# Performance work log

Hardware: AMD Instinct MI355X
Metric: run time of the kernel (lower is better)

Reference implementation:

```python
import jax, jax.numpy as jnp
import numpy as np

# Hyperparameters (from init_kwargs)
D_MODEL = 1024
D_STATE = 64
HEADDIM = 64
MIMO_RANK = 2
CHUNK = 128
EXPAND = 2
D_INNER = EXPAND * D_MODEL            # 2048
NHEADS = D_INNER // HEADDIM           # 32
G = MIMO_RANK * D_STATE               # effective state channels per head = 128
D_CONV = 4
D_XBC = D_INNER + 2 * NHEADS * G      # conv channels
D_IN_PROJ = 2 * D_INNER + 2 * NHEADS * G + NHEADS  # [z, x, B, C, dt]


def rmsnorm(x, w, eps=1e-5):
    return x * w * jax.lax.rsqrt(jnp.mean(x * x, axis=-1, keepdims=True) + eps)


def setup_inputs() -> dict:
    key = jax.random.key(0)
    ks = jax.random.split(key, 8)
    B, L = 2, 2048
    x = jax.random.normal(ks[0], (B, L, D_MODEL), jnp.float32)
    norm_w = jnp.ones((D_MODEL,), jnp.float32)
    in_proj_w = jax.random.normal(ks[1], (D_IN_PROJ, D_MODEL), jnp.float32) * 0.02
    conv_w = jax.random.normal(ks[2], (D_XBC, D_CONV), jnp.float32) * 0.2
    conv_b = jnp.zeros((D_XBC,), jnp.float32)
    dt_bias = jax.random.uniform(ks[3], (NHEADS,), jnp.float32, minval=-4.0, maxval=-1.0)
    A_log = jnp.log(jax.random.uniform(ks[4], (NHEADS,), jnp.float32, minval=1.0, maxval=8.0))
    D_skip = jnp.ones((NHEADS,), jnp.float32)
    gnorm_w = jnp.ones((D_INNER,), jnp.float32)
    out_proj_w = jax.random.normal(ks[5], (D_MODEL, D_INNER), jnp.float32) * 0.02
    return dict(x=x, norm_w=norm_w, in_proj_w=in_proj_w, conv_w=conv_w, conv_b=conv_b,
                dt_bias=dt_bias, A_log=A_log, D_skip=D_skip, gnorm_w=gnorm_w,
                out_proj_w=out_proj_w)


def _mamba3(u, in_proj_w, conv_w, conv_b, dt_bias, A_log, D_skip, gnorm_w, out_proj_w):
    B, L, _ = u.shape
    H, P = NHEADS, HEADDIM
    nc = L // CHUNK

    zxbcdt = u @ in_proj_w.T                                   # (B,L,D_IN_PROJ)
    z, xbc, dt_raw = jnp.split(zxbcdt, [D_INNER, D_INNER + D_XBC], axis=-1)

    # causal depthwise conv (width D_CONV) + SiLU on [x, B, C]
    xp = jnp.pad(xbc, ((0, 0), (D_CONV - 1, 0), (0, 0)))
    conv = conv_b + sum(xp[:, k:k + L, :] * conv_w[:, k] for k in range(D_CONV))
    xbc = jax.nn.silu(conv)
    xh, Bm, Cm = jnp.split(xbc, [D_INNER, D_INNER + H * G], axis=-1)

    Xc = xh.reshape(B, nc, CHUNK, H, P)
    Bc = Bm.reshape(B, nc, CHUNK, H, G)
    Cc = Cm.reshape(B, nc, CHUNK, H, G)

    dt = jax.nn.softplus(dt_raw + dt_bias)                     # (B,L,H), positive
    A = -jnp.exp(A_log)                                        # (H,), negative
    dtc = dt.reshape(B, nc, CHUNK, H)
    a = dtc * A                                                # log decay, (B,nc,cs,H)
    cum = jnp.cumsum(a, axis=2)                                # inclusive cumsum within chunk

    # intra-chunk (quadratic, causal) part
    cumT = cum.transpose(0, 1, 3, 2)                           # (B,nc,H,cs)
    diff = cumT[..., :, None] - cumT[..., None, :]             # cum_l - cum_s
    mask = jnp.tril(jnp.ones((CHUNK, CHUNK), bool))
    decay = jnp.where(mask, jnp.exp(jnp.where(mask, diff, 0.0)), 0.0)
    dtT = dtc.transpose(0, 1, 3, 2)                            # (B,nc,H,cs)
    scores = jnp.einsum('bclhg,bcshg->bchls', Cc, Bc) * decay * dtT[:, :, :, None, :]
    Y_intra = jnp.einsum('bchls,bcshp->bclhp', scores, Xc)

    # inter-chunk state recurrence
    w = jnp.exp(cum[:, :, -1:, :] - cum) * dtc                 # (B,nc,cs,H)
    S = jnp.einsum('bcshg,bcshp->bchgp', Bc * w[..., None], Xc)  # chunk states
    dlast = jnp.exp(cum[:, :, -1, :])                          # (B,nc,H) total chunk decay

    def step(carry, inp):
        dl, s = inp
        return dl[:, :, None, None] * carry + s, carry

    init = jnp.zeros((B, H, G, P), u.dtype)
    _, Hprev = jax.lax.scan(step, init, (dlast.transpose(1, 0, 2), S.transpose(1, 0, 2, 3, 4)))
    Hprev = Hprev.transpose(1, 0, 2, 3, 4)                     # (B,nc,H,G,P) state before chunk
    Y_inter = jnp.einsum('bclhg,bchgp->bclhp', Cc * jnp.exp(cum)[..., None], Hprev)

    y = (Y_intra + Y_inter + D_skip[:, None] * Xc).reshape(B, L, D_INNER)
    y = rmsnorm(y * jax.nn.silu(z), gnorm_w)                   # gated RMSNorm
    return y @ out_proj_w.T


def reference(x, norm_w, in_proj_w, conv_w, conv_b, dt_bias, A_log, D_skip, gnorm_w, out_proj_w):
    # pre-norm residual wrapper
    return x + _mamba3(rmsnorm(x, norm_w), in_proj_w, conv_w, conv_b,
                       dt_bias, A_log, D_skip, gnorm_w, out_proj_w)
```

## Files before the change

### kernel.cpp

```cpp
#include <hip/hip_runtime.h>

typedef unsigned short u16;
typedef __attribute__((ext_vector_type(8))) short bf16x8;
typedef __attribute__((ext_vector_type(4))) float f32x4;

#define MFMA16(a,b,c) __builtin_amdgcn_mfma_f32_16x16x32_bf16(a,b,c,0,0,0)

#define DMODEL   1024
#define DINNER   2048
#define NHEADS   32
#define HEADDIM  64
#define GDIM     128
#define DXBC     10240
#define DPROJ    12320
#define CHUNK_L  128
#define NCHUNK   16
#define NROWS    4096

__device__ __forceinline__ float b2f(u16 u){ return __uint_as_float(((unsigned)u)<<16); }
__device__ __forceinline__ u16 f2b(float f){
  unsigned u = __float_as_uint(f);
  u += 0x7fffu + ((u>>16)&1u);
  return (u16)(u>>16);
}

__device__ __forceinline__ void gload_lds16(const void* g, void* l){
  __builtin_amdgcn_global_load_lds(
      (const __attribute__((address_space(1))) unsigned int*)g,
      (__attribute__((address_space(3))) unsigned int*)l, 16, 0, 0);
}

__global__ void k_f32_to_bf16_2(const float* __restrict__ s1, u16* __restrict__ d1, int n1,
                                const float* __restrict__ s2, u16* __restrict__ d2, int n2){
  int i = blockIdx.x*blockDim.x + threadIdx.x;
  int stride = gridDim.x*blockDim.x;
  int t1 = n1 >> 2, t2 = n2 >> 2;
  for (int j=i; j<t1+t2; j+=stride){
    const float4* sp; uint2* dp; int idx;
    if (j < t1){ sp = (const float4*)s1; dp = (uint2*)d1; idx = j; }
    else       { sp = (const float4*)s2; dp = (uint2*)d2; idx = j - t1; }
    float4 v = sp[idx];
    uint2 o;
    o.x = (unsigned)f2b(v.x) | ((unsigned)f2b(v.y)<<16);
    o.y = (unsigned)f2b(v.z) | ((unsigned)f2b(v.w)<<16);
    dp[idx] = o;
  }
}

__global__ __launch_bounds__(256) void k_rmsnorm_in(const float* __restrict__ x,
                                                    const float* __restrict__ w,
                                                    u16* __restrict__ u){
  int row = blockIdx.x, tid = threadIdx.x;
  float4 v = reinterpret_cast<const float4*>(x + (size_t)row*DMODEL)[tid];
  float ss = v.x*v.x + v.y*v.y + v.z*v.z + v.w*v.w;
  #pragma unroll
  for (int off=32; off>0; off>>=1) ss += __shfl_down(ss, off, 64);
  __shared__ float red[4];
  if ((tid&63)==0) red[tid>>6] = ss;
  __syncthreads();
  float tot = red[0]+red[1]+red[2]+red[3];
  float sc = rsqrtf(tot/(float)DMODEL + 1e-5f);
  float4 wv = reinterpret_cast<const float4*>(w)[tid];
  uint2 o;
  o.x = (unsigned)f2b(v.x*wv.x*sc) | ((unsigned)f2b(v.y*wv.y*sc)<<16);
  o.y = (unsigned)f2b(v.z*wv.z*sc) | ((unsigned)f2b(v.w*wv.w*sc)<<16);
  reinterpret_cast<uint2*>(u + (size_t)row*DMODEL)[tid] = o;
}

__global__ __launch_bounds__(512) void k_gemm1_8p(const u16* __restrict__ A,
                                                  const u16* __restrict__ W,
                                                  u16* __restrict__ zb,
                                                  u16* __restrict__ xbc){
  __shared__ __align__(16) u16 lds[65536];
  const int tid  = threadIdx.x;
  const int lane = tid & 63, w = tid >> 6;
  const int wr = w >> 2, wc = w & 3;
  int bid = blockIdx.x;
  int xcd = bid & 7, g = bid >> 3;
  int st  = xcd*6 + (g >> 4);
  int wi  = g & 15;
  int tm  = (st/12)*4 + (wi>>2);
  int tn  = (st%12)*4 + (wi&3);
  const int m0 = tm*256, n0 = tn*256;

  const int srow = w*8 + (lane>>3);
  const int scol = ((lane&7) ^ ((lane>>3)&7))*8;
  const u16* aS = A + (size_t)(m0 + srow)*DMODEL + scol;
  const u16* bS = W + (size_t)(n0 + srow)*DMODEL + scol;
  const int ldsw = w*512;

  const int rr = lane & 15, gq = lane >> 4;

  f32x4 acc[8][4];
  #pragma unroll
  for (int i=0;i<8;i++)
    #pragma unroll
    for (int j=0;j<4;j++) acc[i][j] = (f32x4){0,0,0,0};

  auto SU_A = [&](int kt, int j){
    gload_lds16(aS + (size_t)(j*64)*DMODEL + kt*64,
                lds + (kt&1)*32768 + j*4096 + ldsw);
  };
  auto SU_B = [&](int kt, int j){
    gload_lds16(bS + (size_t)(j*64)*DMODEL + kt*64,
                lds + (kt&1)*32768 + 16384 + j*4096 + ldsw);
  };

  SU_A(0,0); SU_A(0,2); SU_B(0,0); SU_B(0,2); SU_B(0,1); SU_B(0,3); SU_A(0,1); SU_A(0,3);
  asm volatile("s_waitcnt vmcnt(2)" ::: "memory");
  __builtin_amdgcn_s_barrier();
  __builtin_amdgcn_sched_barrier(0);

  for (int kt = 0; kt < 16; ++kt){
    const u16* bufA = lds + (kt&1)*32768;
    const u16* bufB = bufA + 16384;
    const bool stg = (kt < 15);
    bf16x8 af[4][2], bw0[2][2], bw1[2][2];

    auto RDA = [&](int ti, int ks)->bf16x8{
      int r = wr*128 + ti*16 + rr;
      int s = (ks*4 + gq) ^ (rr & 7);
      return *(const bf16x8*)&bufA[r*64 + s*8];
    };
    auto RDB = [&](int tj, int ks)->bf16x8{
      int r = wc*64 + tj*16 + rr;
      int s = (ks*4 + gq) ^ (rr & 7);
      return *(const bf16x8*)&bufB[r*64 + s*8];
    };

    #pragma unroll
    for (int ti=0;ti<4;ti++){ af[ti][0]=RDA(ti,0); af[ti][1]=RDA(ti,1); }
    #pragma unroll
    for (int tj=0;tj<2;tj++){ bw0[tj][0]=RDB(tj,0); bw0[tj][1]=RDB(tj,1); }
    if (stg){ SU_A(kt+1,0); SU_A(kt+1,2); }
    __builtin_amdgcn_s_barrier();
    asm volatile("s_waitcnt lgkmcnt(0)" ::: "memory");
    __builtin_amdgcn_sched_barrier(0);
    __builtin_amdgcn_s_setprio(1);
    #pragma unroll
    for (int ti=0;ti<4;ti++)
      #pragma unroll
      for (int tj=0;tj<2;tj++){
        acc[ti][tj] = MFMA16(af[ti][0], bw0[tj][0], acc[ti][tj]);
        acc[ti][tj] = MFMA16(af[ti][1], bw0[tj][1], acc[ti][tj]);
      }
    __builtin_amdgcn_s_setprio(0);
    __builtin_amdgcn_s_barrier();

    #pragma unroll
    for (int tj=0;tj<2;tj++){ bw1[tj][0]=RDB(tj+2,0); bw1[tj][1]=RDB(tj+2,1); }
    if (stg){ SU_B(kt+1,0); SU_B(kt+1,2); }
    __builtin_amdgcn_s_barrier();
    asm volatile("s_waitcnt lgkmcnt(0)" ::: "memory");
    __builtin_amdgcn_sched_barrier(0);
    __builtin_amdgcn_s_setprio(1);
    #pragma unroll
    for (int ti=0;ti<4;ti++)
      #pragma unroll
      for (int tj=0;tj<2;tj++){
        acc[ti][tj+2] = MFMA16(af[ti][0], bw1[tj][0], acc[ti][tj+2]);
        acc[ti][tj+2] = MFMA16(af[ti][1], bw1[tj][1], acc[ti][tj+2]);
      }
    __builtin_amdgcn_s_setprio(0);
    if (stg) asm volatile("s_waitcnt vmcnt(4)" ::: "memory");
    else     asm volatile("s_waitcnt vmcnt(0)" ::: "memory");
    __builtin_amdgcn_s_barrier();

    #pragma unroll
    for (int ti=0;ti<4;ti++){ af[ti][0]=RDA(ti+4,0); af[ti][1]=RDA(ti+4,1); }
    if (stg){ SU_B(kt+1,1); SU_B(kt+1,3); }
    __builtin_amdgcn_s_barrier();
    asm volatile("s_waitcnt lgkmcnt(0)" ::: "memory");
    __builtin_amdgcn_sched_barrier(0);
    __builtin_amdgcn_s_setprio(1);
    #pragma unroll
    for (int ti=0;ti<4;ti++)
      #pragma unroll
      for (int tj=0;tj<2;tj++){
        acc[4+ti][tj] = MFMA16(af[ti][0], bw0[tj][0], acc[4+ti][tj]);
        acc[4+ti][tj] = MFMA16(af[ti][1], bw0[tj][1], acc[4+ti][tj]);
      }
    __builtin_amdgcn_s_setprio(0);
    __builtin_amdgcn_s_barrier();

    if (stg){ SU_A(kt+1,1); SU_A(kt+1,3); }
    __builtin_amdgcn_s_barrier();
    __builtin_amdgcn_sched_barrier(0);
    __builtin_amdgcn_s_setprio(1);
    #pragma unroll
    for (int ti=0;ti<4;ti++)
      #pragma unroll
      for (int tj=0;tj<2;tj++){
        acc[4+ti][tj+2] = MFMA16(af[ti][0], bw1[tj][0], acc[4+ti][tj+2]);
        acc[4+ti][tj+2] = MFMA16(af[ti][1], bw1[tj][1], acc[4+ti][tj+2]);
      }
    __builtin_amdgcn_s_setprio(0);
    if (stg){
      asm volatile("s_waitcnt vmcnt(2)" ::: "memory");
      __builtin_amdgcn_s_barrier();
      __builtin_amdgcn_sched_barrier(0);
    }
  }

  const int row0 = m0 + wr*128 + (lane>>4)*4;
  const int colb = wc*64 + (lane&15);
  if (tn >= 8){
    const int cb = n0 - DINNER;
    #pragma unroll
    for (int ti=0;ti<8;ti++)
      #pragma unroll
      for (int tj=0;tj<4;tj++)
        #pragma unroll
        for (int q=0;q<4;q++)
          xbc[(size_t)(row0 + ti*16 + q)*DXBC + cb + colb + tj*16] = f2b(acc[ti][tj][q]);
  } else {
    #pragma unroll
    for (int ti=0;ti<8;ti++)
      #pragma unroll
      for (int tj=0;tj<4;tj++)
        #pragma unroll
        for (int q=0;q<4;q++)
          zb[(size_t)(row0 + ti*16 + q)*DINNER + n0 + colb + tj*16] = f2b(acc[ti][tj][q]);
  }
}

__global__ __launch_bounds__(256) void k_gemm_dt(const u16* __restrict__ A,
                                                 const u16* __restrict__ W,
                                                 float* __restrict__ dtraw){
  const int lane = threadIdx.x & 63, wv = threadIdx.x >> 6;
  const int m0 = blockIdx.x*32;
  const int n0 = DINNER + DXBC;
  const int r  = lane & 15;
  const int kb = (lane>>4)*8;
  const int k0 = wv*256;
  const u16* a0p = A + (size_t)(m0 + r)*DMODEL + k0 + kb;
  const u16* a1p = a0p + 16*DMODEL;
  const u16* b0p = W + (size_t)(n0 + r)*DMODEL + k0 + kb;
  const u16* b1p = b0p + 16*DMODEL;
  f32x4 acc00={0,0,0,0}, acc01={0,0,0,0}, acc10={0,0,0,0}, acc11={0,0,0,0};
  #pragma unroll
  for (int k=0;k<256;k+=32){
    bf16x8 a0 = *(const bf16x8*)(a0p + k);
    bf16x8 a1 = *(const bf16x8*)(a1p + k);
    bf16x8 b0 = *(const bf16x8*)(b0p + k);
    bf16x8 b1 = *(const bf16x8*)(b1p + k);
    acc00 = MFMA16(a0,b0,acc00);
    acc01 = MFMA16(a0,b1,acc01);
    acc10 = MFMA16(a1,b0,acc10);
    acc11 = MFMA16(a1,b1,acc11);
  }
  __shared__ float part[4][1024];
  int rowb = (lane>>4)*4, col = lane&15;
  #pragma unroll
  for (int rr=0; rr<4; rr++){
    part[wv][(rowb+rr)*32 + col]         = acc00[rr];
    part[wv][(rowb+rr)*32 + col+16]      = acc01[rr];
    part[wv][(rowb+16+rr)*32 + col]      = acc10[rr];
    part[wv][(rowb+16+rr)*32 + col+16]   = acc11[rr];
  }
  __syncthreads();
  int idx = threadIdx.x*4;
  #pragma unroll
  for (int q=0;q<4;q++){
    int i = idx+q;
    dtraw[(size_t)m0*NHEADS + i] = part[0][i]+part[1][i]+part[2][i]+part[3][i];
  }
}

__global__ __launch_bounds__(256) void k_conv(const u16* __restrict__ xbc,
                                              const float* __restrict__ cw,
                                              const float* __restrict__ cb,
                                              u16* __restrict__ xh,
                                              u16* __restrict__ Bm,
                                              u16* __restrict__ Cm){
  int c  = (blockIdx.x*256 + threadIdx.x)*2;
  int row0 = blockIdx.y*8;
  int l0 = row0 & 2047;
  float4 wa = reinterpret_cast<const float4*>(cw)[c];
  float4 wb = reinterpret_cast<const float4*>(cw)[c+1];
  float cba = cb[c], cbb = cb[c+1];
  float a3=0,a2=0,a1=0, b3=0,b2=0,b1=0;
  auto loadpair = [&](int rw, float& fa, float& fb){
    unsigned v = *(const unsigned*)&xbc[(size_t)rw*DXBC + c];
    fa = b2f((u16)v); fb = b2f((u16)(v>>16));
  };
  if (l0 >= 3){
    loadpair(row0-3, a3,b3); loadpair(row0-2, a2,b2); loadpair(row0-1, a1,b1);
  }
  #pragma unroll
  for (int i=0;i<8;i++){
    float a0,b0; loadpair(row0+i, a0,b0);
    float sa = cba + a3*wa.x + a2*wa.y + a1*wa.z + a0*wa.w;
    float sb = cbb + b3*wb.x + b2*wb.y + b1*wb.z + b0*wb.w;
    sa = sa/(1.f+expf(-sa)); sb = sb/(1.f+expf(-sb));
    unsigned o = (unsigned)f2b(sa) | ((unsigned)f2b(sb)<<16);
    int rw = row0 + i;
    if (c < DINNER)            *(unsigned*)&xh[(size_t)rw*DINNER + c] = o;
    else if (c < DINNER+4096)  *(unsigned*)&Bm[(size_t)rw*4096 + (c-DINNER)] = o;
    else                       *(unsigned*)&Cm[(size_t)rw*4096 + (c-DINNER-4096)] = o;
    a3=a2; a2=a1; a1=a0; b3=b2; b2=b1; b1=b0;
  }
}

__global__ __launch_bounds__(128) void k_dtscan(const float* __restrict__ dtraw,
                                                const float* __restrict__ dt_bias,
                                                const float* __restrict__ A_log,
                                                float* __restrict__ dtT,
                                                float* __restrict__ cumT){
  int blk = blockIdx.x;
  int h   = blk & 31;
  int bc  = blk >> 5;
  int s   = threadIdx.x;
  int row = bc*128 + s;
  float xv = dtraw[(size_t)row*NHEADS + h] + dt_bias[h];
  float dt = (xv > 20.f) ? xv : log1pf(expf(xv));
  float a  = dt * (-expf(A_log[h]));
  __shared__ float lds[128];
  lds[s] = a; __syncthreads();
  #pragma unroll
  for (int off=1; off<128; off<<=1){
    float t = (s>=off) ? lds[s-off] : 0.f;
    __syncthreads();
    lds[s] += t;
    __syncthreads();
  }
  dtT[(size_t)blk*128 + s]  = dt;
  cumT[(size_t)blk*128 + s] = lds[s];
}

__global__ __launch_bounds__(512) void k_states(const u16* __restrict__ Bm,
                                                const u16* __restrict__ xh,
                                                const float* __restrict__ dtT,
                                                const float* __restrict__ cumT,
                                                u16* __restrict__ S){
  int blk = blockIdx.x;
  int h = blk & 31, bc = blk >> 5;
  __shared__ __align__(16) u16 Bw[128][136];
  __shared__ __align__(16) u16 XT[64][136];
  __shared__ float cum[128], dtv[128];
  int tid = threadIdx.x;
  if (tid < 128){ cum[tid] = cumT[(size_t)blk*128+tid]; dtv[tid] = dtT[(size_t)blk*128+tid]; }
  __syncthreads();
  float clast = cum[127];
  #pragma unroll
  for (int it=0; it<4; ++it){
    int s  = it*32 + (tid>>4);
    int g8 = (tid&15)*8;
    uint4 v = *(const uint4*)&Bm[(size_t)(bc*128+s)*4096 + h*128 + g8];
    float w = expf(clast - cum[s]) * dtv[s];
    const u16* pv = (const u16*)&v;
    #pragma unroll
    for (int j=0;j<8;j++) Bw[g8+j][s] = f2b(b2f(pv[j]) * w);
  }
  #pragma unroll
  for (int it=0; it<4; ++it){
    int s  = it*32 + (tid>>4);
    int p4 = (tid&15)*4;
    uint2 v = *(const uint2*)&xh[(size_t)(bc*128+s)*DINNER + h*64 + p4];
    const u16* pv = (const u16*)&v;
    #pragma unroll
    for (int j=0;j<4;j++) XT[p4+j][s] = pv[j];
  }
  __syncthreads();
  int lane = tid & 63, wv = tid >> 6;
  int r = lane & 15, kb = (lane>>4)*8;
  f32x4 acc[4];
  #pragma unroll
  for (int j=0;j<4;j++) acc[j] = (f32x4){0,0,0,0};
  #pragma unroll
  for (int k=0;k<128;k+=32){
    bf16x8 a0 = *(const bf16x8*)&Bw[wv*16 + r][k+kb];
    #pragma unroll
    for (int tj=0;tj<4;tj++){
      bf16x8 bb = *(const bf16x8*)&XT[tj*16 + r][k+kb];
      acc[tj] = MFMA16(a0,bb,acc[tj]);
    }
  }
  u16* Sp = S + (size_t)blk*8192;
  int g0 = wv*16 + (lane>>4)*4, p0 = lane&15;
  #pragma unroll
  for (int tj=0;tj<4;tj++)
    #pragma unroll
    for (int rr=0;rr<4;rr++)
      Sp[(g0 + rr)*64 + tj*16 + p0] = f2b(acc[tj][rr]);
}

__global__ __launch_bounds__(256) void k_scan(const u16* __restrict__ S,
                                              const float* __restrict__ cumT,
                                              u16* __restrict__ Hp){
  int slice = blockIdx.x & 3;
  int bh = blockIdx.x >> 2;
  int b = bh >> 5, h = bh & 31;
  int e0 = slice*2048 + threadIdx.x*8;
  float c8[8];
  #pragma unroll
  for (int j=0;j<8;j++) c8[j] = 0.f;
  for (int c=0;c<NCHUNK;c++){
    int blk = (b*16+c)*32 + h;
    float dl = expf(cumT[(size_t)blk*128 + 127]);
    uint4 sv = *(const uint4*)&S[(size_t)blk*8192 + e0];
    const u16* sp = (const u16*)&sv;
    uint4 o; u16* op = (u16*)&o;
    #pragma unroll
    for (int j=0;j<8;j++) op[j] = f2b(c8[j]);
    *reinterpret_cast<uint4*>(&Hp[(size_t)blk*8192 + e0]) = o;
    #pragma unroll
    for (int j=0;j<8;j++) c8[j] = dl*c8[j] + b2f(sp[j]);
  }
}

__global__ __launch_bounds__(512) void k_intra(const u16* __restrict__ Cm,
                                               const u16* __restrict__ Bm,
                                               const u16* __restrict__ xh,
                                               const u16* __restrict__ Hp,
                                               const float* __restrict__ dtT,
                                               const float* __restrict__ cumT,
                                               const float* __restrict__ Dskip,
                                               u16* __restrict__ yh){
  int blk = blockIdx.x;
  int h = blk & 31, bc = blk >> 5;
  __shared__ __align__(16) u16 Cl[128][136];
  __shared__ __align__(16) u16 Bl[128][136];
  __shared__ __align__(16) u16 XT[64][136];
  __shared__ __align__(16) u16 HT[64][136];
  __shared__ float cum[128], dtv[128];
  int tid = threadIdx.x;
  if (tid < 128){ cum[tid] = cumT[(size_t)blk*128+tid]; dtv[tid] = dtT[(size_t)blk*128+tid]; }
  #pragma unroll
  for (int it=0; it<4; ++it){
    int rw = it*32 + (tid>>4);
    int g8 = (tid&15)*8;
    *(uint4*)&Cl[rw][g8] = *(const uint4*)&Cm[(size_t)(bc*128+rw)*4096 + h*128 + g8];
    *(uint4*)&Bl[rw][g8] = *(const uint4*)&Bm[(size_t)(bc*128+rw)*4096 + h*128 + g8];
  }
  #pragma unroll
  for (int it=0; it<4; ++it){
    int s  = it*32 + (tid>>4);
    int p4 = (tid&15)*4;
    uint2 v = *(const uint2*)&xh[(size_t)(bc*128+s)*DINNER + h*64 + p4];
    const u16* pv = (const u16*)&v;
    #pragma unroll
    for (int j=0;j<4;j++) XT[p4+j][s] = pv[j];
  }
  #pragma unroll
  for (int it=0; it<4; ++it){
    int g  = it*32 + (tid>>4);
    int p4 = (tid&15)*4;
    uint2 v = *(const uint2*)&Hp[(size_t)blk*8192 + g*64 + p4];
    const u16* pv = (const u16*)&v;
    #pragma unroll
    for (int j=0;j<4;j++) HT[p4+j][g] = pv[j];
  }
  __syncthreads();
  int lane = tid & 63, wv = tid >> 6;
  int r = lane & 15, kb = (lane>>4)*8;
  const int tjmax = wv;

  f32x4 p1[8];
  #pragma unroll
  for (int j=0;j<8;j++) p1[j] = (f32x4){0,0,0,0};
  #pragma unroll
  for (int k=0;k<128;k+=32){
    bf16x8 a0 = *(const bf16x8*)&Cl[wv*16 + r][k+kb];
    #pragma unroll
    for (int tj=0;tj<8;tj++){
      if (tj > tjmax) continue;
      bf16x8 bb = *(const bf16x8*)&Bl[tj*16 + r][k+kb];
      p1[tj] = MFMA16(a0,bb,p1[tj]);
    }
  }
  __syncthreads();
  int row0 = wv*16 + (lane>>4)*4;
  #pragma unroll
  for (int tj=0;tj<8;tj++)
    #pragma unroll
    for (int rr=0;rr<4;rr++){
      int l = row0 + rr;
      int s = tj*16 + (lane&15);
      float v = p1[tj][rr];
      v = (s <= l) ? v * expf(cum[l]-cum[s]) * dtv[s] : 0.f;
      Bl[l][s] = f2b(v);
    }
  __syncthreads();

  f32x4 y[4];
  #pragma unroll
  for (int j=0;j<4;j++) y[j] = (f32x4){0,0,0,0};
  #pragma unroll
  for (int k=0;k<128;k+=32){
    bf16x8 a0 = *(const bf16x8*)&Cl[wv*16 + r][k+kb];
    #pragma unroll
    for (int tj=0;tj<4;tj++){
      bf16x8 bb = *(const bf16x8*)&HT[tj*16 + r][k+kb];
      y[tj] = MFMA16(a0,bb,y[tj]);
    }
  }
  #pragma unroll
  for (int rr=0;rr<4;rr++){
    float e = expf(cum[row0 + rr]);
    #pragma unroll
    for (int tj=0;tj<4;tj++) y[tj][rr] *= e;
  }
  #pragma unroll
  for (int k=0;k<128;k+=32){
    bf16x8 a0 = *(const bf16x8*)&Bl[wv*16 + r][k+kb];
    #pragma unroll
    for (int tj=0;tj<4;tj++){
      bf16x8 bb = *(const bf16x8*)&XT[tj*16 + r][k+kb];
      y[tj] = MFMA16(a0,bb,y[tj]);
    }
  }
  float Dh = Dskip[h];
  #pragma unroll
  for (int tj=0;tj<4;tj++)
    #pragma unroll
    for (int rr=0;rr<4;rr++){
      int l = row0 + rr;
      int p = tj*16 + (lane&15);
      float xv = b2f(XT[p][l]);
      yh[(size_t)(bc*128 + l)*DINNER + h*64 + p] = f2b(y[tj][rr] + Dh*xv);
    }
}

__global__ __launch_bounds__(256) void k_gate(const u16* __restrict__ yh,
                                              const u16* __restrict__ zb,
                                              const float* __restrict__ gw,
                                              u16* __restrict__ out){
  int row = blockIdx.x, tid = threadIdx.x;
  const uint4 yv = reinterpret_cast<const uint4*>(yh + (size_t)row*DINNER)[tid];
  const uint4 zv = reinterpret_cast<const uint4*>(zb + (size_t)row*DINNER)[tid];
  const unsigned* yp = (const unsigned*)&yv;
  const unsigned* zp = (const unsigned*)&zv;
  float t[8]; float ss = 0.f;
  #pragma unroll
  for (int i=0;i<4;i++){
    float y0 = b2f((u16)yp[i]), y1 = b2f((u16)(yp[i]>>16));
    float z0 = b2f((u16)zp[i]), z1 = b2f((u16)(zp[i]>>16));
    float v0 = y0 * (z0 / (1.f + expf(-z0)));
    float v1 = y1 * (z1 / (1.f + expf(-z1)));
    t[2*i] = v0; t[2*i+1] = v1; ss += v0*v0 + v1*v1;
  }
  #pragma unroll
  for (int off=32; off>0; off>>=1) ss += __shfl_down(ss, off, 64);
  __shared__ float red[4];
  if ((tid&63)==0) red[tid>>6] = ss;
  __syncthreads();
  float tot = red[0]+red[1]+red[2]+red[3];
  float g = rsqrtf(tot/(float)DINNER + 1e-5f);
  const float4 g0 = reinterpret_cast<const float4*>(gw)[tid*2];
  const float4 g1 = reinterpret_cast<const float4*>(gw)[tid*2+1];
  uint4 o;
  unsigned* op = (unsigned*)&o;
  float gg[8] = {g0.x,g0.y,g0.z,g0.w,g1.x,g1.y,g1.z,g1.w};
  #pragma unroll
  for (int i=0;i<4;i++)
    op[i] = (unsigned)f2b(t[2*i]*gg[2*i]*g) | ((unsigned)f2b(t[2*i+1]*gg[2*i+1]*g)<<16);
  reinterpret_cast<uint4*>(out + (size_t)row*DINNER)[tid] = o;
}

__global__ __launch_bounds__(256) void k_gemm2_db(const u16* __restrict__ A,
                                                  const u16* __restrict__ W,
                                                  const float* __restrict__ xres,
                                                  float* __restrict__ out){
  __shared__ __align__(16) u16 lds[2*8192];
  const int tid  = threadIdx.x;
  const int lane = tid & 63, wv = tid >> 6;
  const int wr = wv >> 1, wc = wv & 1;
  const int NWG = 8*32, Q = NWG/8;
  int swz = (blockIdx.x & 7)*Q + (blockIdx.x >> 3);
  int tm = swz / 8, tn = swz % 8;
  int m0 = tm*128, n0 = tn*128;

  const int K = DINNER;
  const int srcslot = ((lane&3) ^ ((lane>>3)&3)) * 8;
  const u16* aS0 = A + (size_t)(m0 + wv*32 + (lane>>2))*K + srcslot;
  const u16* aS1 = aS0 + (size_t)16*K;
  const u16* bS0 = W + (size_t)(n0 + wv*32 + (lane>>2))*K + srcslot;
  const u16* bS1 = bS0 + (size_t)16*K;
  const int ldsW = (wv*32)*32;
  const int rr = lane & 15;
  const int kb = (((lane>>4) ^ ((lane>>1)&3))) * 8;

  f32x4 acc[4][4];
  #pragma unroll
  for (int i=0;i<4;i++)
    #pragma unroll
    for (int j=0;j<4;j++) acc[i][j] = (f32x4){0,0,0,0};

  int stage_off = 0;
  auto STAGE = [&](int ks){
    u16* base = lds + (ks&1)*8192;
    gload_lds16(aS0 + stage_off, base + ldsW);
    gload_lds16(aS1 + stage_off, base + 16*32 + ldsW);
    gload_lds16(bS0 + stage_off, base + 4096 + ldsW);
    gload_lds16(bS1 + stage_off, base + 4096 + 16*32 + ldsW);
    stage_off += 32;
  };
  auto KSTEP = [&](int ks, int stage_ks){
    const u16* As = lds + (ks&1)*8192;
    const u16* Bs = As + 4096;
    bf16x8 af[4], bw[4];
    #pragma unroll
    for (int t=0;t<4;t++){
      af[t] = *(const bf16x8*)&As[(wr*64 + t*16 + rr)*32 + kb];
      bw[t] = *(const bf16x8*)&Bs[(wc*64 + t*16 + rr)*32 + kb];
    }
    asm volatile("s_waitcnt lgkmcnt(0)" ::: "memory");
    __builtin_amdgcn_s_barrier();
    if (stage_ks >= 0) STAGE(stage_ks);
    __builtin_amdgcn_s_setprio(1);
    #pragma unroll
    for (int ti=0;ti<4;ti++)
      #pragma unroll
      for (int tj=0;tj<4;tj++)
        acc[ti][tj] = MFMA16(af[ti], bw[tj], acc[ti][tj]);
    __builtin_amdgcn_s_setprio(0);
  };

  STAGE(0); STAGE(1);
  asm volatile("s_waitcnt vmcnt(4)" ::: "memory");
  __builtin_amdgcn_s_barrier();
  __builtin_amdgcn_sched_barrier(0);
  const int NK = K/32;
  for (int ks = 0; ks < NK-2; ++ks){
    KSTEP(ks, ks+2);
    asm volatile("s_waitcnt vmcnt(4)" ::: "memory");
    __builtin_amdgcn_s_barrier();
    __builtin_amdgcn_sched_barrier(0);
  }
  KSTEP(NK-2, -1);
  asm volatile("s_waitcnt vmcnt(0)" ::: "memory");
  __builtin_amdgcn_s_barrier();
  __builtin_amdgcn_sched_barrier(0);
  KSTEP(NK-1, -1);

  int row0 = m0 + wr*64 + (lane>>4)*4;
  int col0 = n0 + wc*64 + (lane&15);
  #pragma unroll
  for (int ti=0;ti<4;ti++)
    #pragma unroll
    for (int tj=0;tj<4;tj++)
      #pragma unroll
      for (int q=0;q<4;q++){
        size_t idx = (size_t)(row0+ti*16+q)*DMODEL + col0 + tj*16;
        out[idx] = acc[ti][tj][q] + xres[idx];
      }
}

extern "C" void kernel_launch(void* const* d_in, const int* in_sizes, int n_in,
                              void* d_out, int out_size, void* d_ws, size_t ws_size,
                              hipStream_t stream) {
  (void)in_sizes; (void)n_in; (void)out_size; (void)ws_size;
  const float* x         = (const float*)d_in[0];
  const float* norm_w    = (const float*)d_in[1];
  const float* in_proj_w = (const float*)d_in[2];
  const float* conv_w    = (const float*)d_in[3];
  const float* conv_b    = (const float*)d_in[4];
  const float* dt_bias   = (const float*)d_in[5];
  const float* A_log     = (const float*)d_in[6];
  const float* D_skip    = (const float*)d_in[7];
  const float* gnorm_w   = (const float*)d_in[8];
  const float* out_proj_w= (const float*)d_in[9];
  float* out = (float*)d_out;

  char* ws = (char*)d_ws;
  size_t off = 0;
  auto alloc = [&](size_t bytes)->char*{
    char* p = ws + off; off = (off + bytes + 255) & ~(size_t)255; return p;
  };
  u16*   W2    = (u16*)  alloc((size_t)DMODEL*DINNER*2);
  u16*   zb    = (u16*)  alloc((size_t)NROWS*DINNER*2);
  float* dtraw = (float*)alloc((size_t)NROWS*NHEADS*4);
  float* dtT   = (float*)alloc((size_t)1024*128*4);
  float* cumT  = (float*)alloc((size_t)1024*128*4);
  u16*   xhb   = (u16*)  alloc((size_t)NROWS*DINNER*2);
  u16*   Bmb   = (u16*)  alloc((size_t)NROWS*4096*2);
  u16*   Cmb   = (u16*)  alloc((size_t)NROWS*4096*2);
  char*  R1    = alloc((size_t)NROWS*DXBC*2);
  u16*   xbcr  = (u16*)R1;
  u16*   S     = (u16*)R1;
  u16*   Hp    = (u16*)(R1 + (size_t)1024*8192*4);
  u16*   yh    = (u16*)R1;
  char*  R2    = alloc((size_t)DPROJ*DMODEL*2 + (size_t)NROWS*DMODEL*2);
  u16*   W1    = (u16*)R2;
  u16*   u_bf  = (u16*)(R2 + (size_t)DPROJ*DMODEL*2);
  u16*   gated = (u16*)R2;

  k_f32_to_bf16_2<<<2048,256,0,stream>>>(in_proj_w, W1, DPROJ*DMODEL,
                                         out_proj_w, W2, DMODEL*DINNER);
  k_rmsnorm_in<<<NROWS,256,0,stream>>>(x, norm_w, u_bf);
  k_gemm1_8p<<<768,512,0,stream>>>(u_bf, W1, zb, xbcr);
  k_gemm_dt<<<NROWS/32,256,0,stream>>>(u_bf, W1, dtraw);
  k_conv<<<dim3(DXBC/512, NROWS/8),256,0,stream>>>(xbcr, conv_w, conv_b, xhb, Bmb, Cmb);
  k_dtscan<<<1024,128,0,stream>>>(dtraw, dt_bias, A_log, dtT, cumT);
  k_states<<<1024,512,0,stream>>>(Bmb, xhb, dtT, cumT, S);
  k_scan<<<256,256,0,stream>>>(S, cumT, Hp);
  k_intra<<<1024,512,0,stream>>>(Cmb, Bmb, xhb, Hp, dtT, cumT, D_skip, yh);
  k_gate<<<NROWS,256,0,stream>>>(yh, zb, gnorm_w, gated);
  k_gemm2_db<<<8*32,256,0,stream>>>(gated, W2, x, out);
}
```

Baseline: 306.0 us.

## Fuse dt GEMM with dt scan, deepen out-proj K tile, register C fragments

Merges the dt projection GEMM and the per-chunk dt softplus/cumsum scan into one kernel with one block per chunk, removing the dtraw round trip and a launch. The output GEMM stages K in tiles of 64 with a new XOR swizzle, halving the number of barrier steps at the cost of larger LDS buffers. k_intra loads C fragments straight into registers instead of staging them through LDS. The conv kernel processes 16 rows per block instead of 8. The fused dt kernel launches only 32 blocks, which leaves most of the GPU idle for that step.

```diff
diff --git a/kernel.cpp b/kernel.cpp
--- a/kernel.cpp
+++ b/kernel.cpp
@@ -224,46 +224,70 @@
   }
 }
 
-__global__ __launch_bounds__(256) void k_gemm_dt(const u16* __restrict__ A,
+__global__ __launch_bounds__(256) void k_dtfused(const u16* __restrict__ A,
                                                  const u16* __restrict__ W,
-                                                 float* __restrict__ dtraw){
-  const int lane = threadIdx.x & 63, wv = threadIdx.x >> 6;
-  const int m0 = blockIdx.x*32;
-  const int n0 = DINNER + DXBC;
-  const int r  = lane & 15;
-  const int kb = (lane>>4)*8;
+                                                 const float* __restrict__ dt_bias,
+                                                 const float* __restrict__ A_log,
+                                                 float* __restrict__ dtT,
+                                                 float* __restrict__ cumT){
+  __shared__ float part[4][128][33];
+  const int bc = blockIdx.x;
+  const int tid = threadIdx.x;
+  const int lane = tid & 63, wv = tid >> 6;
+  const int r = lane & 15, kb = (lane>>4)*8;
   const int k0 = wv*256;
-  const u16* a0p = A + (size_t)(m0 + r)*DMODEL + k0 + kb;
-  const u16* a1p = a0p + 16*DMODEL;
-  const u16* b0p = W + (size_t)(n0 + r)*DMODEL + k0 + kb;
-  const u16* b1p = b0p + 16*DMODEL;
-  f32x4 acc00={0,0,0,0}, acc01={0,0,0,0}, acc10={0,0,0,0}, acc11={0,0,0,0};
-  #pragma unroll
-  for (int k=0;k<256;k+=32){
-    bf16x8 a0 = *(const bf16x8*)(a0p + k);
-    bf16x8 a1 = *(const bf16x8*)(a1p + k);
-    bf16x8 b0 = *(const bf16x8*)(b0p + k);
-    bf16x8 b1 = *(const bf16x8*)(b1p + k);
-    acc00 = MFMA16(a0,b0,acc00);
-    acc01 = MFMA16(a0,b1,acc01);
-    acc10 = MFMA16(a1,b0,acc10);
-    acc11 = MFMA16(a1,b1,acc11);
-  }
-  __shared__ float part[4][1024];
-  int rowb = (lane>>4)*4, col = lane&15;
-  #pragma unroll
-  for (int rr=0; rr<4; rr++){
-    part[wv][(rowb+rr)*32 + col]         = acc00[rr];
-    part[wv][(rowb+rr)*32 + col+16]      = acc01[rr];
-    part[wv][(rowb+16+rr)*32 + col]      = acc10[rr];
-    part[wv][(rowb+16+rr)*32 + col+16]   = acc11[rr];
-  }
-  __syncthreads();
-  int idx = threadIdx.x*4;
-  #pragma unroll
-  for (int q=0;q<4;q++){
-    int i = idx+q;
-    dtraw[(size_t)m0*NHEADS + i] = part[0][i]+part[1][i]+part[2][i]+part[3][i];
+  const u16* b0p = W + (size_t)(12288 + r)*DMODEL + k0 + kb;
+  const u16* b1p = b0p + (size_t)16*DMODEL;
+  f32x4 acc[8][2];
+  #pragma unroll
+  for (int t=0;t<8;t++){ acc[t][0]=(f32x4){0,0,0,0}; acc[t][1]=(f32x4){0,0,0,0}; }
+  #pragma unroll
+  for (int ks=0; ks<256; ks+=32){
+    bf16x8 b0 = *(const bf16x8*)(b0p + ks);
+    bf16x8 b1 = *(const bf16x8*)(b1p + ks);
+    #pragma unroll
+    for (int ti=0;ti<8;ti++){
+      bf16x8 a = *(const bf16x8*)(A + (size_t)(bc*128 + ti*16 + r)*DMODEL + k0 + kb + ks);
+      acc[ti][0] = MFMA16(a,b0,acc[ti][0]);
+      acc[ti][1] = MFMA16(a,b1,acc[ti][1]);
+    }
+  }
+  #pragma unroll
+  for (int ti=0;ti<8;ti++)
+    #pragma unroll
+    for (int cj=0;cj<2;cj++)
+      #pragma unroll
+      for (int q=0;q<4;q++)
+        part[wv][ti*16 + (lane>>4)*4 + q][cj*16 + (lane&15)] = acc[ti][cj][q];
+  __syncthreads();
+  for (int i = tid; i < 128*32; i += 256){
+    int s = i >> 5, h = i & 31;
+    float v = part[0][s][h]+part[1][s][h]+part[2][s][h]+part[3][s][h] + dt_bias[h];
+    float dt = (v > 20.f) ? v : log1pf(expf(v));
+    part[0][s][h] = dt;
+    part[1][s][h] = dt * (-expf(A_log[h]));
+  }
+  __syncthreads();
+  #pragma unroll
+  for (int off=1; off<128; off<<=1){
+    float t[16];
+    #pragma unroll
+    for (int j=0;j<16;j++){
+      int i = tid + j*256; int s = i>>5, h = i&31;
+      t[j] = (s>=off) ? part[1][s-off][h] : 0.f;
+    }
+    __syncthreads();
+    #pragma unroll
+    for (int j=0;j<16;j++){
+      int i = tid + j*256; int s = i>>5, h = i&31;
+      part[1][s][h] += t[j];
+    }
+    __syncthreads();
+  }
+  for (int i = tid; i < 4096; i += 256){
+    int h = i >> 7, s = i & 127;
+    dtT [((size_t)bc*32 + h)*128 + s] = part[0][s][h];
+    cumT[((size_t)bc*32 + h)*128 + s] = part[1][s][h];
   }
 }
 
@@ -274,7 +298,7 @@
                                               u16* __restrict__ Bm,
                                               u16* __restrict__ Cm){
   int c  = (blockIdx.x*256 + threadIdx.x)*2;
-  int row0 = blockIdx.y*8;
+  int row0 = blockIdx.y*16;
   int l0 = row0 & 2047;
   float4 wa = reinterpret_cast<const float4*>(cw)[c];
   float4 wb = reinterpret_cast<const float4*>(cw)[c+1];
@@ -288,7 +312,7 @@
     loadpair(row0-3, a3,b3); loadpair(row0-2, a2,b2); loadpair(row0-1, a1,b1);
   }
   #pragma unroll
-  for (int i=0;i<8;i++){
+  for (int i=0;i<16;i++){
     float a0,b0; loadpair(row0+i, a0,b0);
     float sa = cba + a3*wa.x + a2*wa.y + a1*wa.z + a0*wa.w;
     float sb = cbb + b3*wb.x + b2*wb.y + b1*wb.z + b0*wb.w;
@@ -300,32 +324,6 @@
     else                       *(unsigned*)&Cm[(size_t)rw*4096 + (c-DINNER-4096)] = o;
     a3=a2; a2=a1; a1=a0; b3=b2; b2=b1; b1=b0;
   }
-}
-
-__global__ __launch_bounds__(128) void k_dtscan(const float* __restrict__ dtraw,
-                                                const float* __restrict__ dt_bias,
-                                                const float* __restrict__ A_log,
-                                                float* __restrict__ dtT,
-                                                float* __restrict__ cumT){
-  int blk = blockIdx.x;
-  int h   = blk & 31;
-  int bc  = blk >> 5;
-  int s   = threadIdx.x;
-  int row = bc*128 + s;
-  float xv = dtraw[(size_t)row*NHEADS + h] + dt_bias[h];
-  float dt = (xv > 20.f) ? xv : log1pf(expf(xv));
-  float a  = dt * (-expf(A_log[h]));
-  __shared__ float lds[128];
-  lds[s] = a; __syncthreads();
-  #pragma unroll
-  for (int off=1; off<128; off<<=1){
-    float t = (s>=off) ? lds[s-off] : 0.f;
-    __syncthreads();
-    lds[s] += t;
-    __syncthreads();
-  }
-  dtT[(size_t)blk*128 + s]  = dt;
-  cumT[(size_t)blk*128 + s] = lds[s];
 }
 
 __global__ __launch_bounds__(512) void k_states(const u16* __restrict__ Bm,
@@ -419,18 +417,26 @@
                                                u16* __restrict__ yh){
   int blk = blockIdx.x;
   int h = blk & 31, bc = blk >> 5;
-  __shared__ __align__(16) u16 Cl[128][136];
   __shared__ __align__(16) u16 Bl[128][136];
   __shared__ __align__(16) u16 XT[64][136];
   __shared__ __align__(16) u16 HT[64][136];
   __shared__ float cum[128], dtv[128];
   int tid = threadIdx.x;
+  int lane = tid & 63, wv = tid >> 6;
+  int r = lane & 15, kb = (lane>>4)*8;
+
+  bf16x8 cfr[4];
+  {
+    const u16* cp = Cm + (size_t)(bc*128 + wv*16 + r)*4096 + h*128 + kb;
+    #pragma unroll
+    for (int ks=0;ks<4;ks++) cfr[ks] = *(const bf16x8*)(cp + ks*32);
+  }
+
   if (tid < 128){ cum[tid] = cumT[(size_t)blk*128+tid]; dtv[tid] = dtT[(size_t)blk*128+tid]; }
   #pragma unroll
   for (int it=0; it<4; ++it){
     int rw = it*32 + (tid>>4);
     int g8 = (tid&15)*8;
-    *(uint4*)&Cl[rw][g8] = *(const uint4*)&Cm[(size_t)(bc*128+rw)*4096 + h*128 + g8];
     *(uint4*)&Bl[rw][g8] = *(const uint4*)&Bm[(size_t)(bc*128+rw)*4096 + h*128 + g8];
   }
   #pragma unroll
@@ -452,20 +458,18 @@
     for (int j=0;j<4;j++) HT[p4+j][g] = pv[j];
   }
   __syncthreads();
-  int lane = tid & 63, wv = tid >> 6;
-  int r = lane & 15, kb = (lane>>4)*8;
   const int tjmax = wv;
 
   f32x4 p1[8];
   #pragma unroll
   for (int j=0;j<8;j++) p1[j] = (f32x4){0,0,0,0};
   #pragma unroll
-  for (int k=0;k<128;k+=32){
-    bf16x8 a0 = *(const bf16x8*)&Cl[wv*16 + r][k+kb];
+  for (int ks=0;ks<4;ks++){
+    bf16x8 a0 = cfr[ks];
     #pragma unroll
     for (int tj=0;tj<8;tj++){
       if (tj > tjmax) continue;
-      bf16x8 bb = *(const bf16x8*)&Bl[tj*16 + r][k+kb];
+      bf16x8 bb = *(const bf16x8*)&Bl[tj*16 + r][ks*32+kb];
       p1[tj] = MFMA16(a0,bb,p1[tj]);
     }
   }
@@ -487,11 +491,11 @@
   #pragma unroll
   for (int j=0;j<4;j++) y[j] = (f32x4){0,0,0,0};
   #pragma unroll
-  for (int k=0;k<128;k+=32){
-    bf16x8 a0 = *(const bf16x8*)&Cl[wv*16 + r][k+kb];
+  for (int ks=0;ks<4;ks++){
+    bf16x8 a0 = cfr[ks];
     #pragma unroll
     for (int tj=0;tj<4;tj++){
-      bf16x8 bb = *(const bf16x8*)&HT[tj*16 + r][k+kb];
+      bf16x8 bb = *(const bf16x8*)&HT[tj*16 + r][ks*32+kb];
       y[tj] = MFMA16(a0,bb,y[tj]);
     }
   }
@@ -558,11 +562,11 @@
   reinterpret_cast<uint4*>(out + (size_t)row*DINNER)[tid] = o;
 }
 
-__global__ __launch_bounds__(256) void k_gemm2_db(const u16* __restrict__ A,
+__global__ __launch_bounds__(256) void k_gemm2_64(const u16* __restrict__ A,
                                                   const u16* __restrict__ W,
                                                   const float* __restrict__ xres,
                                                   float* __restrict__ out){
-  __shared__ __align__(16) u16 lds[2*8192];
+  __shared__ __align__(16) u16 lds[2*16384];
   const int tid  = threadIdx.x;
   const int lane = tid & 63, wv = tid >> 6;
   const int wr = wv >> 1, wc = wv & 1;
@@ -570,16 +574,15 @@
   int swz = (blockIdx.x & 7)*Q + (blockIdx.x >> 3);
   int tm = swz / 8, tn = swz % 8;
   int m0 = tm*128, n0 = tn*128;
-
   const int K = DINNER;
-  const int srcslot = ((lane&3) ^ ((lane>>3)&3)) * 8;
-  const u16* aS0 = A + (size_t)(m0 + wv*32 + (lane>>2))*K + srcslot;
-  const u16* aS1 = aS0 + (size_t)16*K;
-  const u16* bS0 = W + (size_t)(n0 + wv*32 + (lane>>2))*K + srcslot;
-  const u16* bS1 = bS0 + (size_t)16*K;
-  const int ldsW = (wv*32)*32;
-  const int rr = lane & 15;
-  const int kb = (((lane>>4) ^ ((lane>>1)&3))) * 8;
+
+  const int srow = tid >> 3;
+  const int sslot = ((tid&7) ^ ((tid>>3)&7))*8;
+  const u16* aSrc = A + (size_t)(m0 + srow)*K + sslot;
+  const u16* bSrc = W + (size_t)(n0 + srow)*K + sslot;
+  const int ldsu = wv*512;
+
+  const int rr = lane & 15, gq = lane >> 4;
 
   f32x4 acc[4][4];
   #pragma unroll
@@ -587,52 +590,58 @@
     #pragma unroll
     for (int j=0;j<4;j++) acc[i][j] = (f32x4){0,0,0,0};
 
-  int stage_off = 0;
-  auto STAGE = [&](int ks){
-    u16* base = lds + (ks&1)*8192;
-    gload_lds16(aS0 + stage_off, base + ldsW);
-    gload_lds16(aS1 + stage_off, base + 16*32 + ldsW);
-    gload_lds16(bS0 + stage_off, base + 4096 + ldsW);
-    gload_lds16(bS1 + stage_off, base + 4096 + 16*32 + ldsW);
-    stage_off += 32;
+  auto STAGE = [&](int kt){
+    u16* base = lds + (kt&1)*16384;
+    #pragma unroll
+    for (int j=0;j<4;j++)
+      gload_lds16(aSrc + (size_t)(j*32)*K + kt*64, base + j*2048 + ldsu);
+    #pragma unroll
+    for (int j=0;j<4;j++)
+      gload_lds16(bSrc + (size_t)(j*32)*K + kt*64, base + 8192 + j*2048 + ldsu);
   };
-  auto KSTEP = [&](int ks, int stage_ks){
-    const u16* As = lds + (ks&1)*8192;
-    const u16* Bs = As + 4096;
-    bf16x8 af[4], bw[4];
+  auto KSTEP = [&](int kt, bool stg){
+    const u16* bufA = lds + (kt&1)*16384;
+    const u16* bufB = bufA + 8192;
+    bf16x8 af[4][2], bw[4][2];
     #pragma unroll
     for (int t=0;t<4;t++){
-      af[t] = *(const bf16x8*)&As[(wr*64 + t*16 + rr)*32 + kb];
-      bw[t] = *(const bf16x8*)&Bs[(wc*64 + t*16 + rr)*32 + kb];
+      #pragma unroll
+      for (int ks=0;ks<2;ks++){
+        int sa = (ks*4 + gq) ^ (rr & 7);
+        af[t][ks] = *(const bf16x8*)&bufA[(wr*64 + t*16 + rr)*64 + sa*8];
+        bw[t][ks] = *(const bf16x8*)&bufB[(wc*64 + t*16 + rr)*64 + sa*8];
+      }
     }
     asm volatile("s_waitcnt lgkmcnt(0)" ::: "memory");
     __builtin_amdgcn_s_barrier();
-    if (stage_ks >= 0) STAGE(stage_ks);
+    if (stg) STAGE(kt+2);
     __builtin_amdgcn_s_setprio(1);
     #pragma unroll
     for (int ti=0;ti<4;ti++)
       #pragma unroll
-      for (int tj=0;tj<4;tj++)
-        acc[ti][tj] = MFMA16(af[ti], bw[tj], acc[ti][tj]);
+      for (int tj=0;tj<4;tj++){
+        acc[ti][tj] = MFMA16(af[ti][0], bw[tj][0], acc[ti][tj]);
+        acc[ti][tj] = MFMA16(af[ti][1], bw[tj][1], acc[ti][tj]);
+      }
     __builtin_amdgcn_s_setprio(0);
   };
 
   STAGE(0); STAGE(1);
-  asm volatile("s_waitcnt vmcnt(4)" ::: "memory");
+  asm volatile("s_waitcnt vmcnt(8)" ::: "memory");
   __builtin_amdgcn_s_barrier();
   __builtin_amdgcn_sched_barrier(0);
-  const int NK = K/32;
-  for (int ks = 0; ks < NK-2; ++ks){
-    KSTEP(ks, ks+2);
-    asm volatile("s_waitcnt vmcnt(4)" ::: "memory");
+  const int NT = K/64;
+  for (int kt = 0; kt < NT-2; ++kt){
+    KSTEP(kt, true);
+    asm volatile("s_waitcnt vmcnt(8)" ::: "memory");
     __builtin_amdgcn_s_barrier();
     __builtin_amdgcn_sched_barrier(0);
   }
-  KSTEP(NK-2, -1);
+  KSTEP(NT-2, false);
   asm volatile("s_waitcnt vmcnt(0)" ::: "memory");
   __builtin_amdgcn_s_barrier();
   __builtin_amdgcn_sched_barrier(0);
-  KSTEP(NK-1, -1);
+  KSTEP(NT-1, false);
 
   int row0 = m0 + wr*64 + (lane>>4)*4;
   int col0 = n0 + wc*64 + (lane&15);
@@ -670,7 +679,6 @@
   };
   u16*   W2    = (u16*)  alloc((size_t)DMODEL*DINNER*2);
   u16*   zb    = (u16*)  alloc((size_t)NROWS*DINNER*2);
-  float* dtraw = (float*)alloc((size_t)NROWS*NHEADS*4);
   float* dtT   = (float*)alloc((size_t)1024*128*4);
   float* cumT  = (float*)alloc((size_t)1024*128*4);
   u16*   xhb   = (u16*)  alloc((size_t)NROWS*DINNER*2);
@@ -690,12 +698,11 @@
                                          out_proj_w, W2, DMODEL*DINNER);
   k_rmsnorm_in<<<NROWS,256,0,stream>>>(x, norm_w, u_bf);
   k_gemm1_8p<<<768,512,0,stream>>>(u_bf, W1, zb, xbcr);
-  k_gemm_dt<<<NROWS/32,256,0,stream>>>(u_bf, W1, dtraw);
-  k_conv<<<dim3(DXBC/512, NROWS/8),256,0,stream>>>(xbcr, conv_w, conv_b, xhb, Bmb, Cmb);
-  k_dtscan<<<1024,128,0,stream>>>(dtraw, dt_bias, A_log, dtT, cumT);
+  k_dtfused<<<32,256,0,stream>>>(u_bf, W1, dt_bias, A_log, dtT, cumT);
+  k_conv<<<dim3(DXBC/512, NROWS/16),256,0,stream>>>(xbcr, conv_w, conv_b, xhb, Bmb, Cmb);
   k_states<<<1024,512,0,stream>>>(Bmb, xhb, dtT, cumT, S);
   k_scan<<<256,256,0,stream>>>(S, cumT, Hp);
   k_intra<<<1024,512,0,stream>>>(Cmb, Bmb, xhb, Hp, dtT, cumT, D_skip, yh);
   k_gate<<<NROWS,256,0,stream>>>(yh, zb, gnorm_w, gated);
-  k_gemm2_db<<<8*32,256,0,stream>>>(gated, W2, x, out);
-}
+  k_gemm2_64<<<8*32,256,0,stream>>>(gated, W2, x, out);
+}
```

Measured after the change: 310.3 us. About the same (+1.4%).
